# Performance work log

Hardware: AMD Instinct MI355X
Metric: run time of the kernel (lower is better)

Reference implementation:

```python
import jax, jax.numpy as jnp
import numpy as np

B, S, H = 1, 2048, 2048
NH, NOPE, ROPE, VHD = 16, 128, 64, 128
QHD = NOPE + ROPE            # 192
QLR, KVLR, FF = 1536, 512, 8192
SCALE = QHD ** -0.5          # rope_scaling is None -> mscale = 1
EPS = 1e-6
THETA = 10000.0


def _rms(x, w):
    return x * jax.lax.rsqrt(jnp.mean(x * x, axis=-1, keepdims=True) + EPS) * w


def _rotate_half(x):
    x1, x2 = x[..., : x.shape[-1] // 2], x[..., x.shape[-1] // 2 :]
    return jnp.concatenate((-x2, x1), axis=-1)


def _rope(x, cos, sin, pos):
    # x: (b, h, s, d). First de-interleave pairs: (even dims | odd dims),
    # matching the reshape/transpose in apply_rotary_pos_emb.
    b, h, s, d = x.shape
    x = x.reshape(b, h, s, d // 2, 2).transpose(0, 1, 2, 4, 3).reshape(b, h, s, d)
    c = cos[pos][:, None]   # (b, 1, s, d)
    sn = sin[pos][:, None]
    return x * c + _rotate_half(x) * sn


def setup_inputs() -> dict:
    key = jax.random.key(0)
    ks = jax.random.split(key, 10)
    w = lambda k, shp: jax.random.normal(k, shp, jnp.float32) * 0.02
    hidden_states = jax.random.normal(ks[0], (B, S, H), jnp.float32)
    position_ids = jnp.tile(jnp.arange(S, dtype=jnp.int32)[None], (B, 1))
    inv_freq = 1.0 / (THETA ** (jnp.arange(0, ROPE, 2, dtype=jnp.float32) / ROPE))
    freqs = jnp.arange(S, dtype=jnp.float32)[:, None] * inv_freq[None, :]
    emb = jnp.concatenate([freqs, freqs], axis=-1)  # (S, ROPE)
    return {
        "hidden_states": hidden_states,
        "sin": jnp.sin(emb),
        "cos": jnp.cos(emb),
        "wq_a": w(ks[1], (H, QLR)),
        "q_a_ln": jnp.ones((QLR,), jnp.float32),
        "wq_b": w(ks[2], (QLR, NH * QHD)),
        "wkv_a": w(ks[3], (H, KVLR + ROPE)),
        "kv_a_ln": jnp.ones((KVLR,), jnp.float32),
        "wkv_b": w(ks[4], (KVLR, NH * (NOPE + VHD))),
        "wo": w(ks[5], (NH * VHD, H)),
        "in_ln": jnp.ones((H,), jnp.float32),
        "post_ln": jnp.ones((H,), jnp.float32),
        "w_gate": w(ks[6], (H, FF)),
        "w_up": w(ks[7], (H, FF)),
        "w_down": w(ks[8], (FF, H)),
        "position_ids": position_ids,
    }


def reference(hidden_states, sin, cos, wq_a, q_a_ln, wq_b, wkv_a, kv_a_ln,
              wkv_b, wo, in_ln, post_ln, w_gate, w_up, w_down, position_ids):
    residual = hidden_states
    x = _rms(hidden_states, in_ln)

    # --- MLA: low-rank Q ---
    q = _rms(x @ wq_a, q_a_ln) @ wq_b                       # (B,S,NH*QHD)
    q = q.reshape(B, S, NH, QHD).transpose(0, 2, 1, 3)      # (B,NH,S,QHD)
    q_nope, q_pe = q[..., :NOPE], q[..., NOPE:]

    # --- low-rank KV with shared (MQA) rope key ---
    ckv = x @ wkv_a                                          # (B,S,KVLR+ROPE)
    k_pe = ckv[..., KVLR:].reshape(B, S, 1, ROPE).transpose(0, 2, 1, 3)
    kv = (_rms(ckv[..., :KVLR], kv_a_ln) @ wkv_b)
    kv = kv.reshape(B, S, NH, NOPE + VHD).transpose(0, 2, 1, 3)
    k_nope, v = kv[..., :NOPE], kv[..., NOPE:]

    q_pe = _rope(q_pe, cos, sin, position_ids)
    k_pe = _rope(k_pe, cos, sin, position_ids)

    qs = jnp.concatenate([q_nope, q_pe], axis=-1)            # (B,NH,S,QHD)
    ks = jnp.concatenate([k_nope, jnp.broadcast_to(k_pe, (B, NH, S, ROPE))], axis=-1)

    scores = jnp.einsum("bhqd,bhkd->bhqk", qs, ks) * SCALE
    causal = jnp.tril(jnp.ones((S, S), bool))
    scores = jnp.where(causal, scores, jnp.finfo(scores.dtype).min)
    attn = jax.nn.softmax(scores, axis=-1)
    out = jnp.einsum("bhqk,bhkd->bhqd", attn, v)
    out = out.transpose(0, 2, 1, 3).reshape(B, S, NH * VHD)
    hidden = residual + out @ wo

    # --- dense gated-SiLU MLP ---
    residual = hidden
    y = _rms(hidden, post_ln)
    mlp = (jax.nn.silu(y @ w_gate) * (y @ w_up)) @ w_down
    return residual + mlp
```

## Files before the change

kernel.cpp:

```cpp
#include <hip/hip_runtime.h>
#include <math.h>

#define ATTN_SCALE 0.07216878364870322f

typedef __attribute__((ext_vector_type(8))) short short8;
typedef __attribute__((ext_vector_type(4))) float floatx4;

__device__ __forceinline__ unsigned short f2bf(float f) {
    union { float f; unsigned int u; } v; v.f = f;
    unsigned int r = v.u + 0x7fffu + ((v.u >> 16) & 1u);
    return (unsigned short)(r >> 16);
}
__device__ __forceinline__ float bf2f(unsigned short h) {
    union { unsigned int u; float f; } v; v.u = ((unsigned int)h) << 16;
    return v.f;
}
__device__ __forceinline__ void gld16(const void* g, void* l) {
    __builtin_amdgcn_global_load_lds(
        (const __attribute__((address_space(1))) unsigned int*)g,
        (__attribute__((address_space(3))) unsigned int*)l, 16, 0, 0);
}

__global__ __launch_bounds__(256) void rms_kernel(
    const float* __restrict__ in, int ld_in,
    const float* __restrict__ w,
    unsigned short* __restrict__ out, int ld_out, int N)
{
    const int row = blockIdx.x;
    const int tid = threadIdx.x;
    const float* x = in + (size_t)row * ld_in;
    float ss = 0.f;
    for (int i = tid * 4; i < N; i += 1024) {
        float4 v = *(const float4*)(x + i);
        ss += v.x * v.x + v.y * v.y + v.z * v.z + v.w * v.w;
    }
    #pragma unroll
    for (int off = 32; off > 0; off >>= 1)
        ss += __shfl_down(ss, off);
    __shared__ float red[4];
    const int lane = tid & 63, wid = tid >> 6;
    if (lane == 0) red[wid] = ss;
    __syncthreads();
    const float tot = red[0] + red[1] + red[2] + red[3];
    const float rs = rsqrtf(tot / (float)N + 1e-6f);
    unsigned short* o = out + (size_t)row * ld_out;
    for (int i = tid * 4; i < N; i += 1024) {
        float4 v = *(const float4*)(x + i);
        float4 wv = *(const float4*)(w + i);
        __align__(8) unsigned short ov[4];
        ov[0] = f2bf(v.x * rs * wv.x);
        ov[1] = f2bf(v.y * rs * wv.y);
        ov[2] = f2bf(v.z * rs * wv.z);
        ov[3] = f2bf(v.w * rs * wv.w);
        *(uint2*)&o[i] = *(uint2*)ov;
    }
}

__global__ __launch_bounds__(256) void cast_transpose_kernel(
    const float* __restrict__ W, unsigned short* __restrict__ Wt,
    int K, int N)
{
    __shared__ float tile[64][65];
    const int tid = threadIdx.x;
    const int kb = blockIdx.y * 64;
    const int nb = blockIdx.x * 64;
    const int r  = tid >> 2;
    const int c0 = (tid & 3) * 16;
    if (nb + 64 <= N) {
        #pragma unroll
        for (int j = 0; j < 16; j += 4)
            *(float4*)&tile[r][c0 + j] =
                *(const float4*)&W[(size_t)(kb + r) * N + nb + c0 + j];
    } else {
        for (int j = 0; j < 16; ++j) {
            int n = nb + c0 + j;
            tile[r][c0 + j] = (n < N) ? W[(size_t)(kb + r) * N + n] : 0.f;
        }
    }
    __syncthreads();
    __align__(16) unsigned short ov[16];
    #pragma unroll
    for (int j = 0; j < 16; ++j) ov[j] = f2bf(tile[c0 + j][r]);
    int4* dst = (int4*)&Wt[(size_t)(nb + r) * K + kb + c0];
    dst[0] = ((int4*)ov)[0];
    dst[1] = ((int4*)ov)[1];
}

__global__ __launch_bounds__(256) void gemm_bf16_kernel(
    const unsigned short* __restrict__ A,
    const unsigned short* __restrict__ Bt,
    float* __restrict__ C,
    unsigned short* __restrict__ Cb,
    const float* __restrict__ R,
    int N, int K)
{
    __shared__ __align__(16) unsigned short As[2][4096];
    __shared__ __align__(16) unsigned short Bs[2][4096];
    const int tid = threadIdx.x;
    const int w  = tid >> 6;
    const int l  = tid & 63;
    const int lm = l & 15;
    const int lk = l >> 4;
    const int row0 = blockIdx.y * 128;
    const int col0 = blockIdx.x * 128;
    const int wm = (w >> 1) * 64;
    const int wn = (w & 1) * 64;
    const int nsplit = gridDim.z;
    const int kz = blockIdx.z;
    const int kchunk = K / nsplit;
    const int kbase = kz * kchunk;

    const unsigned short* a0 = A  + (size_t)(row0 + w * 16 + lm) * K + kbase + lk * 8;
    const unsigned short* a1 = a0 + (size_t)64 * K;
    const unsigned short* b0 = Bt + (size_t)(col0 + w * 16 + lm) * K + kbase + lk * 8;
    const unsigned short* b1 = b0 + (size_t)64 * K;
    const int s0 = w * 512 + l * 8;
    const int s1 = (w + 4) * 512 + l * 8;

    floatx4 acc[4][4];
    #pragma unroll
    for (int i = 0; i < 4; ++i)
        #pragma unroll
        for (int j = 0; j < 4; ++j)
            acc[i][j] = (floatx4){0.f, 0.f, 0.f, 0.f};

    gld16(a0, &As[0][s0]);
    gld16(a1, &As[0][s1]);
    gld16(b0, &Bs[0][s0]);
    gld16(b1, &Bs[0][s1]);
    a0 += 32; a1 += 32; b0 += 32; b1 += 32;
    __syncthreads();

    const int niter = kchunk >> 5;
    int cur = 0;
    for (int t = 0; t < niter; ++t) {
        if (t + 1 < niter) {
            gld16(a0, &As[cur ^ 1][s0]);
            gld16(a1, &As[cur ^ 1][s1]);
            gld16(b0, &Bs[cur ^ 1][s0]);
            gld16(b1, &Bs[cur ^ 1][s1]);
            a0 += 32; a1 += 32; b0 += 32; b1 += 32;
        }
        short8 af[4], bg_[4];
        #pragma unroll
        for (int i = 0; i < 4; ++i)
            af[i] = *(const short8*)&As[cur][((w >> 1) * 4 + i) * 512 + l * 8];
        #pragma unroll
        for (int j = 0; j < 4; ++j)
            bg_[j] = *(const short8*)&Bs[cur][((w & 1) * 4 + j) * 512 + l * 8];
        #pragma unroll
        for (int i = 0; i < 4; ++i)
            #pragma unroll
            for (int j = 0; j < 4; ++j)
                acc[i][j] = __builtin_amdgcn_mfma_f32_16x16x32_bf16(
                    af[i], bg_[j], acc[i][j], 0, 0, 0);
        __syncthreads();
        cur ^= 1;
    }

    const int quad = l >> 4;
    const bool ng = (col0 + 128 > N);
    #pragma unroll
    for (int i = 0; i < 4; ++i) {
        #pragma unroll
        for (int r = 0; r < 4; ++r) {
            const int m = row0 + wm + i * 16 + quad * 4 + r;
            #pragma unroll
            for (int j = 0; j < 4; ++j) {
                const int n = col0 + wn + j * 16 + lm;
                if (ng && n >= N) continue;
                const size_t off = (size_t)m * N + n;
                float v = acc[i][j][r];
                if (nsplit > 1) {
                    if (R && kz == 0) v += R[off];
                    unsafeAtomicAdd(&C[off], v);
                } else if (Cb) {
                    Cb[off] = f2bf(v);
                } else {
                    if (R) v += R[off];
                    C[off] = v;
                }
            }
        }
    }
}

__global__ __launch_bounds__(256) void rope_q_kernel(
    unsigned short* __restrict__ x,
    const float* __restrict__ cosb, const float* __restrict__ sinb,
    const int* __restrict__ pos_ids)
{
    const int gid = blockIdx.x * 256 + threadIdx.x;
    const int i = gid & 31;
    const int grp = gid >> 5;
    const int hh = grp & 15;
    const int row = grp >> 4;
    unsigned short* base = x + (size_t)row * 3072 + hh * 192 + 128;
    const float x0 = bf2f(base[2 * i]);
    const float x1 = bf2f(base[2 * i + 1]);
    const int p = pos_ids[row];
    const float c = cosb[p * 64 + i];
    const float s = sinb[p * 64 + i];
    __syncthreads();
    base[i]      = f2bf(x0 * c - x1 * s);
    base[32 + i] = f2bf(x1 * c + x0 * s);
}

__global__ __launch_bounds__(256) void rope_kpe_kernel(
    const float* __restrict__ ckv, unsigned short* __restrict__ kpe,
    const float* __restrict__ cosb, const float* __restrict__ sinb,
    const int* __restrict__ pos_ids)
{
    const int gid = blockIdx.x * 256 + threadIdx.x;
    const int i = gid & 31;
    const int row = gid >> 5;
    const float x0 = ckv[(size_t)row * 576 + 512 + 2 * i];
    const float x1 = ckv[(size_t)row * 576 + 512 + 2 * i + 1];
    const int p = pos_ids[row];
    const float c = cosb[p * 64 + i];
    const float s = sinb[p * 64 + i];
    kpe[(size_t)row * 64 + i]      = f2bf(x0 * c - x1 * s);
    kpe[(size_t)row * 64 + 32 + i] = f2bf(x1 * c + x0 * s);
}

__global__ __launch_bounds__(256) void vtrans_kernel(
    const unsigned short* __restrict__ kvb, unsigned short* __restrict__ vtg)
{
    __shared__ unsigned short tile[64][72];
    const int tid = threadIdx.x;
    const int s0 = blockIdx.x * 64;
    const int d0 = blockIdx.y * 64;
    const int h  = blockIdx.z;
    const int r  = tid >> 2;
    const int c0 = (tid & 3) * 16;
    *(int4*)&tile[r][c0] =
        *(const int4*)&kvb[(size_t)(s0 + r) * 4096 + h * 256 + 128 + d0 + c0];
    *(int4*)&tile[r][c0 + 8] =
        *(const int4*)&kvb[(size_t)(s0 + r) * 4096 + h * 256 + 128 + d0 + c0 + 8];
    __syncthreads();
    __align__(16) unsigned short ov[16];
    #pragma unroll
    for (int j = 0; j < 16; ++j) ov[j] = tile[c0 + j][r];
    unsigned short* dst = vtg + ((size_t)(h * 128 + d0 + r)) * 2048 + s0 + c0;
    ((int4*)dst)[0] = ((int4*)ov)[0];
    ((int4*)dst)[1] = ((int4*)ov)[1];
}

__global__ __launch_bounds__(512) void attn_mfma_kernel(
    const unsigned short* __restrict__ qb,
    const unsigned short* __restrict__ kvb,
    const unsigned short* __restrict__ kpe,
    const unsigned short* __restrict__ vtg,
    unsigned short* __restrict__ out)
{
    __shared__ __align__(16) unsigned short Kf[128 * 200];
    __shared__ __align__(16) unsigned short Vt[2][128 * 136];
    __shared__ __align__(16) unsigned short Ps[64 * 136];
    __shared__ float pmax_s[8][64];
    __shared__ float psum_s[8][64];
    __shared__ __align__(16) float m_state[64];
    __shared__ __align__(16) float l_state[64];
    __shared__ __align__(16) float alpha_s[64];
    __shared__ __align__(16) float mnew_s[64];

    const int tid  = threadIdx.x;
    const int w    = tid >> 6;
    const int l    = tid & 63;
    const int l15  = l & 15;
    const int quad = l >> 4;
    const int h    = blockIdx.y;
    const int qs   = (w & 3) * 16;
    const int dh   = (w >> 2) * 64;

    for (int pass = 0; pass < 2; ++pass) {
        const int qt = pass ? (31 - (int)blockIdx.x) : (int)blockIdx.x;
        const int q0 = qt * 64;
        const int ntiles = (qt >> 1) + 1;

        short8 qf[4][6];
        #pragma unroll
        for (int nt = 0; nt < 4; ++nt)
            #pragma unroll
            for (int c = 0; c < 6; ++c)
                qf[nt][c] = *(const short8*)&qb[(size_t)(q0 + nt * 16 + l15) * 3072
                                               + h * 192 + c * 32 + quad * 8];

        floatx4 oacc[4];
        #pragma unroll
        for (int nt = 0; nt < 4; ++nt) oacc[nt] = (floatx4){0.f, 0.f, 0.f, 0.f};
        if (tid < 64) { m_state[tid] = -3e38f; l_state[tid] = 0.f; }

        {
            const int k0 = 0;
            for (int s = w; s < 50; s += 8) {
                unsigned ab = s * 1024 + l * 16;
                unsigned row = ab / 400u;
                unsigned g = (ab - row * 400u) >> 4;
                const unsigned short* src;
                if (g < 16u)      src = kvb + (size_t)(k0 + row) * 4096 + h * 256 + g * 8;
                else if (g < 24u) src = kpe + (size_t)(k0 + row) * 64 + (g - 16u) * 8;
                else              src = kpe + (size_t)(k0 + row) * 64;
                gld16(src, (char*)Kf + ab);
            }
            for (int s = w; s < 34; s += 8) {
                unsigned ab = s * 1024 + l * 16;
                unsigned row = ab / 272u;
                unsigned g = (ab - row * 272u) >> 4;
                const unsigned short* src =
                    vtg + (size_t)(h * 128 + row) * 2048 + k0 + (g < 16u ? g * 8 : 0u);
                gld16(src, (char*)Vt[0] + ab);
            }
        }

        for (int kt = 0; kt < ntiles; ++kt) {
            const int k0 = kt * 128;
            const int vb = kt & 1;
            __syncthreads();

            floatx4 st[4];
            #pragma unroll
            for (int nt = 0; nt < 4; ++nt) st[nt] = (floatx4){0.f, 0.f, 0.f, 0.f};
            #pragma unroll
            for (int c = 0; c < 6; ++c) {
                short8 kf = *(const short8*)&Kf[(w * 16 + l15) * 200 + c * 32 + quad * 8];
                #pragma unroll
                for (int nt = 0; nt < 4; ++nt)
                    st[nt] = __builtin_amdgcn_mfma_f32_16x16x32_bf16(kf, qf[nt][c], st[nt], 0, 0, 0);
            }
            #pragma unroll
            for (int nt = 0; nt < 4; ++nt) {
                const int qq = q0 + nt * 16 + l15;
                float vmax = -3e38f;
                #pragma unroll
                for (int r = 0; r < 4; ++r) {
                    const int kpos = k0 + w * 16 + quad * 4 + r;
                    float v = st[nt][r] * ATTN_SCALE;
                    if (kpos > qq) v = -3e38f;
                    st[nt][r] = v;
                    vmax = fmaxf(vmax, v);
                }
                vmax = fmaxf(vmax, __shfl_xor(vmax, 16));
                vmax = fmaxf(vmax, __shfl_xor(vmax, 32));
                if (quad == 0) pmax_s[w][nt * 16 + l15] = vmax;
            }
            __syncthreads();
            if (tid < 64) {
                float mp = m_state[tid];
                float mn = mp;
                #pragma unroll
                for (int ww = 0; ww < 8; ++ww) mn = fmaxf(mn, pmax_s[ww][tid]);
                alpha_s[tid] = __expf(mp - mn);
                mnew_s[tid] = mn;
                m_state[tid] = mn;
            }
            __syncthreads();

            #pragma unroll
            for (int nt = 0; nt < 4; ++nt) {
                const float mn = mnew_s[nt * 16 + l15];
                float vsum = 0.f;
                __align__(8) unsigned short pb[4];
                #pragma unroll
                for (int r = 0; r < 4; ++r) {
                    float p = __expf(st[nt][r] - mn);
                    vsum += p;
                    pb[r] = f2bf(p);
                }
                *(uint2*)&Ps[(nt * 16 + l15) * 136 + w * 16 + quad * 4] = *(uint2*)pb;
                vsum += __shfl_xor(vsum, 16);
                vsum += __shfl_xor(vsum, 32);
                if (quad == 0) psum_s[w][nt * 16 + l15] = vsum;
            }
            {
                float4 al4 = *(const float4*)&alpha_s[qs + quad * 4];
                #pragma unroll
                for (int nt = 0; nt < 4; ++nt) {
                    oacc[nt][0] *= al4.x; oacc[nt][1] *= al4.y;
                    oacc[nt][2] *= al4.z; oacc[nt][3] *= al4.w;
                }
            }
            __syncthreads();
            if (tid < 64) {
                float acc = 0.f;
                #pragma unroll
                for (int ww = 0; ww < 8; ++ww) acc += psum_s[ww][tid];
                l_state[tid] = l_state[tid] * alpha_s[tid] + acc;
            }
            if (kt + 1 < ntiles) {
                const int k1 = k0 + 128;
                for (int s = w; s < 50; s += 8) {
                    unsigned ab = s * 1024 + l * 16;
                    unsigned row = ab / 400u;
                    unsigned g = (ab - row * 400u) >> 4;
                    const unsigned short* src;
                    if (g < 16u)      src = kvb + (size_t)(k1 + row) * 4096 + h * 256 + g * 8;
                    else if (g < 24u) src = kpe + (size_t)(k1 + row) * 64 + (g - 16u) * 8;
                    else              src = kpe + (size_t)(k1 + row) * 64;
                    gld16(src, (char*)Kf + ab);
                }
                for (int s = w; s < 34; s += 8) {
                    unsigned ab = s * 1024 + l * 16;
                    unsigned row = ab / 272u;
                    unsigned g = (ab - row * 272u) >> 4;
                    const unsigned short* src =
                        vtg + (size_t)(h * 128 + row) * 2048 + k1 + (g < 16u ? g * 8 : 0u);
                    gld16(src, (char*)Vt[vb ^ 1] + ab);
                }
            }
            #pragma unroll
            for (int c = 0; c < 4; ++c) {
                short8 pf = *(const short8*)&Ps[(qs + l15) * 136 + c * 32 + quad * 8];
                #pragma unroll
                for (int nt = 0; nt < 4; ++nt) {
                    short8 vf = *(const short8*)&Vt[vb][(dh + nt * 16 + l15) * 136
                                                       + c * 32 + quad * 8];
                    oacc[nt] = __builtin_amdgcn_mfma_f32_16x16x32_bf16(pf, vf, oacc[nt], 0, 0, 0);
                }
            }
        }
        __syncthreads();

        {
            float4 l4 = *(const float4*)&l_state[qs + quad * 4];
            float inv0 = 1.f / l4.x, inv1 = 1.f / l4.y, inv2 = 1.f / l4.z, inv3 = 1.f / l4.w;
            #pragma unroll
            for (int nt = 0; nt < 4; ++nt) {
                const size_t col = h * 128 + dh + nt * 16 + l15;
                out[(size_t)(q0 + qs + quad * 4 + 0) * 2048 + col] = f2bf(oacc[nt][0] * inv0);
                out[(size_t)(q0 + qs + quad * 4 + 1) * 2048 + col] = f2bf(oacc[nt][1] * inv1);
                out[(size_t)(q0 + qs + quad * 4 + 2) * 2048 + col] = f2bf(oacc[nt][2] * inv2);
                out[(size_t)(q0 + qs + quad * 4 + 3) * 2048 + col] = f2bf(oacc[nt][3] * inv3);
            }
        }
        __syncthreads();
    }
}

__global__ __launch_bounds__(256) void silu_mul_kernel(
    unsigned short* __restrict__ g, const unsigned short* __restrict__ u, int n8)
{
    int i = blockIdx.x * 256 + threadIdx.x;
    if (i >= n8) return;
    int4 gv = ((const int4*)g)[i];
    int4 uv = ((const int4*)u)[i];
    const unsigned short* gs = (const unsigned short*)&gv;
    const unsigned short* us = (const unsigned short*)&uv;
    __align__(16) unsigned short ov[8];
    #pragma unroll
    for (int j = 0; j < 8; ++j) {
        float gf = bf2f(gs[j]), uf = bf2f(us[j]);
        ov[j] = f2bf(gf * uf / (1.f + __expf(-gf)));
    }
    ((int4*)g)[i] = *(int4*)ov;
}

extern "C" void kernel_launch(void* const* d_in, const int* in_sizes, int n_in,
                              void* d_out, int out_size, void* d_ws, size_t ws_size,
                              hipStream_t stream)
{
    (void)in_sizes; (void)n_in; (void)out_size; (void)ws_size;
    const float* hidden  = (const float*)d_in[0];
    const float* sinb    = (const float*)d_in[1];
    const float* cosb    = (const float*)d_in[2];
    const float* wq_a    = (const float*)d_in[3];
    const float* q_a_ln  = (const float*)d_in[4];
    const float* wq_b    = (const float*)d_in[5];
    const float* wkv_a   = (const float*)d_in[6];
    const float* kv_a_ln = (const float*)d_in[7];
    const float* wkv_b   = (const float*)d_in[8];
    const float* wo      = (const float*)d_in[9];
    const float* in_ln   = (const float*)d_in[10];
    const float* post_ln = (const float*)d_in[11];
    const float* w_gate  = (const float*)d_in[12];
    const float* w_up    = (const float*)d_in[13];
    const float* w_down  = (const float*)d_in[14];
    const int*   pos     = (const int*)d_in[15];

    char* wsb = (char*)d_ws;
    size_t used = 0;
    auto alloc = [&](size_t bytes) {
        char* p = wsb + used;
        used += (bytes + 255) & ~(size_t)255;
        return p;
    };
    float* q_a   = (float*)alloc((size_t)2048 * 1536 * 4);
    float* ckv   = (float*)alloc((size_t)2048 * 576 * 4);
    float* h2    = (float*)alloc((size_t)2048 * 2048 * 4);
    unsigned short* xnb  = (unsigned short*)alloc((size_t)2048 * 2048 * 2);
    unsigned short* qab  = (unsigned short*)alloc((size_t)2048 * 1536 * 2);
    unsigned short* kvnb = (unsigned short*)alloc((size_t)2048 * 512 * 2);
    unsigned short* qbb  = (unsigned short*)alloc((size_t)2048 * 3072 * 2);
    unsigned short* kvbb = (unsigned short*)alloc((size_t)2048 * 4096 * 2);
    unsigned short* kpe  = (unsigned short*)alloc((size_t)2048 * 64 * 2);
    unsigned short* vtg  = (unsigned short*)alloc((size_t)16 * 128 * 2048 * 2);
    unsigned short* attb = (unsigned short*)alloc((size_t)2048 * 2048 * 2);
    unsigned short* gb   = (unsigned short*)alloc((size_t)2048 * 8192 * 2);
    unsigned short* ub   = (unsigned short*)alloc((size_t)2048 * 8192 * 2);
    unsigned short* wt   = (unsigned short*)alloc((size_t)16777216 * 2);
    float* outp = (float*)d_out;

    hipMemsetAsync(q_a, 0, (size_t)2048 * 1536 * 4, stream);
    hipMemsetAsync(ckv, 0, (size_t)2048 * 576 * 4, stream);
    hipMemsetAsync(h2, 0, (size_t)2048 * 2048 * 4, stream);
    hipMemsetAsync(outp, 0, (size_t)2048 * 2048 * 4, stream);

    rms_kernel<<<2048, 256, 0, stream>>>(hidden, 2048, in_ln, xnb, 2048, 2048);
    cast_transpose_kernel<<<dim3(24, 32), 256, 0, stream>>>(wq_a, wt, 2048, 1536);
    gemm_bf16_kernel<<<dim3(12, 16, 2), 256, 0, stream>>>(xnb, wt, q_a, nullptr, nullptr, 1536, 2048);
    rms_kernel<<<2048, 256, 0, stream>>>(q_a, 1536, q_a_ln, qab, 1536, 1536);
    cast_transpose_kernel<<<dim3(48, 24), 256, 0, stream>>>(wq_b, wt, 1536, 3072);
    gemm_bf16_kernel<<<dim3(24, 16), 256, 0, stream>>>(qab, wt, nullptr, qbb, nullptr, 3072, 1536);
    cast_transpose_kernel<<<dim3(10, 32), 256, 0, stream>>>(wkv_a, wt, 2048, 576);
    gemm_bf16_kernel<<<dim3(5, 16, 4), 256, 0, stream>>>(xnb, wt, ckv, nullptr, nullptr, 576, 2048);
    rms_kernel<<<2048, 256, 0, stream>>>(ckv, 576, kv_a_ln, kvnb, 512, 512);
    cast_transpose_kernel<<<dim3(64, 8), 256, 0, stream>>>(wkv_b, wt, 512, 4096);
    gemm_bf16_kernel<<<dim3(32, 16), 256, 0, stream>>>(kvnb, wt, nullptr, kvbb, nullptr, 4096, 512);
    rope_q_kernel<<<4096, 256, 0, stream>>>(qbb, cosb, sinb, pos);
    rope_kpe_kernel<<<256, 256, 0, stream>>>(ckv, kpe, cosb, sinb, pos);
    vtrans_kernel<<<dim3(32, 2, 16), 256, 0, stream>>>(kvbb, vtg);
    attn_mfma_kernel<<<dim3(16, 16), 512, 0, stream>>>(qbb, kvbb, kpe, vtg, attb);
    cast_transpose_kernel<<<dim3(32, 32), 256, 0, stream>>>(wo, wt, 2048, 2048);
    gemm_bf16_kernel<<<dim3(16, 16, 2), 256, 0, stream>>>(attb, wt, h2, nullptr, hidden, 2048, 2048);
    rms_kernel<<<2048, 256, 0, stream>>>(h2, 2048, post_ln, xnb, 2048, 2048);
    cast_transpose_kernel<<<dim3(128, 32), 256, 0, stream>>>(w_gate, wt, 2048, 8192);
    gemm_bf16_kernel<<<dim3(64, 16), 256, 0, stream>>>(xnb, wt, nullptr, gb, nullptr, 8192, 2048);
    cast_transpose_kernel<<<dim3(128, 32), 256, 0, stream>>>(w_up, wt, 2048, 8192);
    gemm_bf16_kernel<<<dim3(64, 16), 256, 0, stream>>>(xnb, wt, nullptr, ub, nullptr, 8192, 2048);
    silu_mul_kernel<<<8192, 256, 0, stream>>>(gb, ub, 2097152);
    cast_transpose_kernel<<<dim3(32, 128), 256, 0, stream>>>(w_down, wt, 8192, 2048);
    gemm_bf16_kernel<<<dim3(16, 16, 4), 256, 0, stream>>>(gb, wt, outp, nullptr, h2, 2048, 8192);
}
```

Measured before the change: 1.144 ms.

## Add 256x256-tile bf16 GEMM kernel for output projection and MLP GEMMs

Introduces a new 512-thread GEMM kernel that computes 256x256 output tiles per workgroup with double-buffered direct-to-LDS loads, XCD-aware block remapping, and MFMA priority hints. It replaces the 128-tile GEMM for the wo projection and the three MLP GEMMs, aiming to raise arithmetic intensity and cut global/LDS traffic per FLOP. The larger tile uses 128 KB of LDS and many accumulator registers, which limits occupancy. Grids are small (64–256 workgroups), so wave-level parallelism drops on the large GPU.

```diff
diff --git a/kernel.cpp b/kernel.cpp
--- a/kernel.cpp
+++ b/kernel.cpp
@@ -169,6 +169,125 @@
             for (int j = 0; j < 4; ++j) {
                 const int n = col0 + wn + j * 16 + lm;
                 if (ng && n >= N) continue;
+                const size_t off = (size_t)m * N + n;
+                float v = acc[i][j][r];
+                if (nsplit > 1) {
+                    if (R && kz == 0) v += R[off];
+                    unsafeAtomicAdd(&C[off], v);
+                } else if (Cb) {
+                    Cb[off] = f2bf(v);
+                } else {
+                    if (R) v += R[off];
+                    C[off] = v;
+                }
+            }
+        }
+    }
+}
+
+__global__ __launch_bounds__(512) void gemm256_kernel(
+    const unsigned short* __restrict__ A,
+    const unsigned short* __restrict__ Bt,
+    float* __restrict__ C,
+    unsigned short* __restrict__ Cb,
+    const float* __restrict__ R,
+    int N, int K)
+{
+    __shared__ __align__(16) unsigned short As[2][16384];
+    __shared__ __align__(16) unsigned short Bs[2][16384];
+    const int tid = threadIdx.x;
+    const int w   = tid >> 6;
+    const int l   = tid & 63;
+    const int lm  = l & 15;
+    const int quad = l >> 4;
+    const int wm2 = w >> 2;
+    const int wn4 = w & 3;
+
+    const int gx = gridDim.x;
+    const int nwg = gx * gridDim.y;
+    int bid = blockIdx.y * gx + blockIdx.x;
+    {
+        const int q = nwg >> 3, r = nwg & 7;
+        const int xcd = bid & 7, off = bid >> 3;
+        bid = (xcd < r ? xcd * (q + 1) : r * (q + 1) + (xcd - r) * q) + off;
+    }
+    const int row0 = (bid / gx) * 256;
+    const int col0 = (bid % gx) * 256;
+
+    const int nsplit = gridDim.z;
+    const int kz = blockIdx.z;
+    const int kchunk = K / nsplit;
+    const int kbase = kz * kchunk;
+
+    const int slk = (tid >> 4) & 7;
+    const int srg = tid >> 7;
+    const unsigned short* sa = A  + (size_t)(row0 + srg * 16 + lm) * K + kbase + slk * 8;
+    const unsigned short* sb = Bt + (size_t)(col0 + srg * 16 + lm) * K + kbase + slk * 8;
+
+    floatx4 acc[8][4];
+    #pragma unroll
+    for (int i = 0; i < 8; ++i)
+        #pragma unroll
+        for (int j = 0; j < 4; ++j)
+            acc[i][j] = (floatx4){0.f, 0.f, 0.f, 0.f};
+
+    const int nt = kchunk >> 6;
+    #pragma unroll
+    for (int j = 0; j < 4; ++j) {
+        gld16(sa + (size_t)j * 64 * K, (char*)As[0] + j * 8192 + tid * 16);
+        gld16(sb + (size_t)j * 64 * K, (char*)Bs[0] + j * 8192 + tid * 16);
+    }
+
+    for (int t = 0; t < nt; ++t) {
+        const int cur = t & 1;
+        if (t + 1 < nt) {
+            const size_t ko = (size_t)(t + 1) * 64;
+            #pragma unroll
+            for (int j = 0; j < 4; ++j) {
+                gld16(sa + (size_t)j * 64 * K + ko, (char*)As[cur ^ 1] + j * 8192 + tid * 16);
+                gld16(sb + (size_t)j * 64 * K + ko, (char*)Bs[cur ^ 1] + j * 8192 + tid * 16);
+            }
+            asm volatile("s_waitcnt vmcnt(8)" ::: "memory");
+        } else {
+            asm volatile("s_waitcnt vmcnt(0)" ::: "memory");
+        }
+        __builtin_amdgcn_sched_barrier(0);
+        __builtin_amdgcn_s_barrier();
+        __builtin_amdgcn_sched_barrier(0);
+
+        const char* ab = (const char*)As[cur] + wm2 * 16384 + l * 16;
+        const char* bb = (const char*)Bs[cur] + wn4 * 8192  + l * 16;
+        #pragma unroll
+        for (int c = 0; c < 2; ++c) {
+            short8 af[8], bf[4];
+            #pragma unroll
+            for (int i = 0; i < 8; ++i)
+                af[i] = *(const short8*)(ab + i * 2048 + c * 1024);
+            #pragma unroll
+            for (int j = 0; j < 4; ++j)
+                bf[j] = *(const short8*)(bb + j * 2048 + c * 1024);
+            __builtin_amdgcn_s_setprio(1);
+            #pragma unroll
+            for (int i = 0; i < 8; ++i)
+                #pragma unroll
+                for (int j = 0; j < 4; ++j)
+                    acc[i][j] = __builtin_amdgcn_mfma_f32_16x16x32_bf16(
+                        af[i], bf[j], acc[i][j], 0, 0, 0);
+            __builtin_amdgcn_s_setprio(0);
+        }
+        __builtin_amdgcn_sched_barrier(0);
+        __builtin_amdgcn_s_barrier();
+        __builtin_amdgcn_sched_barrier(0);
+    }
+
+    #pragma unroll
+    for (int i = 0; i < 8; ++i) {
+        #pragma unroll
+        for (int r = 0; r < 4; ++r) {
+            const int m = row0 + wm2 * 128 + i * 16 + quad * 4 + r;
+            #pragma unroll
+            for (int j = 0; j < 4; ++j) {
+                const int n = col0 + wn4 * 64 + j * 16 + lm;
                 const size_t off = (size_t)m * N + n;
                 float v = acc[i][j][r];
                 if (nsplit > 1) {
@@ -520,13 +639,13 @@
     vtrans_kernel<<<dim3(32, 2, 16), 256, 0, stream>>>(kvbb, vtg);
     attn_mfma_kernel<<<dim3(16, 16), 512, 0, stream>>>(qbb, kvbb, kpe, vtg, attb);
     cast_transpose_kernel<<<dim3(32, 32), 256, 0, stream>>>(wo, wt, 2048, 2048);
-    gemm_bf16_kernel<<<dim3(16, 16, 2), 256, 0, stream>>>(attb, wt, h2, nullptr, hidden, 2048, 2048);
+    gemm256_kernel<<<dim3(8, 8, 4), 512, 0, stream>>>(attb, wt, h2, nullptr, hidden, 2048, 2048);
     rms_kernel<<<2048, 256, 0, stream>>>(h2, 2048, post_ln, xnb, 2048, 2048);
     cast_transpose_kernel<<<dim3(128, 32), 256, 0, stream>>>(w_gate, wt, 2048, 8192);
-    gemm_bf16_kernel<<<dim3(64, 16), 256, 0, stream>>>(xnb, wt, nullptr, gb, nullptr, 8192, 2048);
+    gemm256_kernel<<<dim3(32, 8, 1), 512, 0, stream>>>(xnb, wt, nullptr, gb, nullptr, 8192, 2048);
     cast_transpose_kernel<<<dim3(128, 32), 256, 0, stream>>>(w_up, wt, 2048, 8192);
-    gemm_bf16_kernel<<<dim3(64, 16), 256, 0, stream>>>(xnb, wt, nullptr, ub, nullptr, 8192, 2048);
+    gemm256_kernel<<<dim3(32, 8, 1), 512, 0, stream>>>(xnb, wt, nullptr, ub, nullptr, 8192, 2048);
     silu_mul_kernel<<<8192, 256, 0, stream>>>(gb, ub, 2097152);
     cast_transpose_kernel<<<dim3(32, 128), 256, 0, stream>>>(w_down, wt, 8192, 2048);
-    gemm_bf16_kernel<<<dim3(16, 16, 4), 256, 0, stream>>>(gb, wt, outp, nullptr, h2, 2048, 8192);
-}
+    gemm256_kernel<<<dim3(8, 8, 4), 512, 0, stream>>>(gb, wt, outp, nullptr, h2, 2048, 8192);
+}
```

Result: faster. 1.067 ms (-6.8%).
